# Kernel tuning notes

Hardware: AMD Instinct MI355X
Metric: run time of the kernel (lower is better)

## Reference

```python
import jax, jax.numpy as jnp
import numpy as np

B_SCALE = 1.3195079565048218
N_LEVELS = 16
BASE_RES = 16
MAX_PARAMS = 2 ** 19
N_POINTS = 1048576
PRIMES = (1, 2654435761, 805459861)  # uint32 hash primes (Instant-NGP)


def _level_meta():
    offsets, sizes, inds = [], [], []
    off = 0
    for i in range(N_LEVELS):
        res = int(np.ceil(BASE_RES * np.exp(i * np.log(B_SCALE)) - 1.0)) + 1
        p = res ** 3
        if p % 8 != 0:
            p = ((p + 7) // 8) * 8
        p = min(MAX_PARAMS, p)
        offsets.append(off)
        sizes.append(p)
        inds.append(res ** 3 <= p)  # dense (under_hash) vs hashed level
        off += p
    return offsets, sizes, inds, off


OFFSETS, SIZES, INDICATORS, TOTAL_PARAMS = _level_meta()
TOTAL_HASH_SIZE = TOTAL_PARAMS * 2  # == 11445040


def _encode_level(x01, table2, level):
    # x01: [N,3] in [0,1]; table2: [total_params, 2]
    scale = np.float32(BASE_RES * np.exp(level * np.log(B_SCALE)) - 1.0)
    resolution = np.uint32(np.ceil(scale) + 1)
    map_size = np.uint32(SIZES[level])
    pos = x01 * scale + 0.5
    grid_f = jnp.floor(pos)
    frac = pos - grid_f                           # [N,3] trilinear weights
    grid = grid_f.astype(jnp.uint32)              # [N,3]
    feat = jnp.zeros((x01.shape[0], 2), dtype=table2.dtype)
    primes = np.array(PRIMES, dtype=np.uint32)
    stride = np.array([1, int(resolution), int(resolution) * int(resolution)], dtype=np.uint32)
    for idx in range(8):  # 8 grid corners
        sel = np.array([(idx >> d) & 1 for d in range(3)], dtype=np.uint32)
        corner = grid + sel                       # [N,3] uint32
        w = jnp.prod(jnp.where(sel[None, :] == 1, frac, 1.0 - frac), axis=-1)  # [N]
        if INDICATORS[level]:
            c = corner * stride[None, :]
            h = c[:, 0] + c[:, 1] + c[:, 2]       # under_hash (dense indexing)
        else:
            c = corner * primes[None, :]          # uint32 wraparound multiply
            h = c[:, 0] ^ c[:, 1] ^ c[:, 2]       # fast_hash
        index = (h % map_size).astype(jnp.int32) + np.int32(OFFSETS[level])
        feat = feat + w[:, None] * table2[index]  # gather + trilinear blend
    return feat


def setup_inputs() -> dict:
    key = jax.random.key(0)
    k1, k2 = jax.random.split(key)
    positions = jax.random.uniform(k1, (N_POINTS, 3), dtype=jnp.float32, minval=-1.0, maxval=1.0)
    # random_initialize: (rand*2-1)*1e-4
    hash_table = jax.random.uniform(k2, (TOTAL_HASH_SIZE,), dtype=jnp.float32, minval=-1e-4, maxval=1e-4)
    return {"positions": positions, "hash_table": hash_table}


def reference(positions, hash_table):
    x01 = (positions + 1.0) * 0.5  # bound = 1
    table2 = hash_table.reshape(-1, 2)
    feats = [_encode_level(x01, table2, l) for l in range(N_LEVELS)]
    return jnp.concatenate(feats, axis=-1)  # [N, 32]
```

## Files before the change

kernel.cpp:

```cpp
#include <hip/hip_runtime.h>
#include <math.h>
#include <stdint.h>

#define NLV 16
#define NDENSE 6
#define NHASH 10
#define SORT_RES 32
#define NBINS (SORT_RES * SORT_RES * SORT_RES)

typedef float evf2 __attribute__((ext_vector_type(2)));
typedef unsigned int evu4 __attribute__((ext_vector_type(4)));

struct Params {
  float scale[NLV];
  uint32_t res[NLV];
  uint32_t msize[NLV];
  uint32_t offset[NLV];
};

struct ParamsD {
  float scale[NDENSE];
  uint32_t res[NDENSE];
  uint32_t msize[NDENSE];
  uint32_t offset[NDENSE];
};

__device__ __forceinline__ float ntload(const float* p) {
  return __builtin_nontemporal_load(p);
}

__device__ __forceinline__ uint32_t cell_key(float xr, float yr, float zr) {
  float x01 = (xr + 1.0f) * 0.5f;
  float y01 = (yr + 1.0f) * 0.5f;
  float z01 = (zr + 1.0f) * 0.5f;
  int cx = (int)(x01 * (float)SORT_RES);
  int cy = (int)(y01 * (float)SORT_RES);
  int cz = (int)(z01 * (float)SORT_RES);
  cx = cx < 0 ? 0 : (cx > SORT_RES-1 ? SORT_RES-1 : cx);
  cy = cy < 0 ? 0 : (cy > SORT_RES-1 ? SORT_RES-1 : cy);
  cz = cz < 0 ? 0 : (cz > SORT_RES-1 ? SORT_RES-1 : cz);
  return (uint32_t)(cx | (cy << 5) | (cz << 10));
}

__global__ __launch_bounds__(256) void zero_bins_kernel(uint32_t* bins) {
  int i = blockIdx.x * 256 + threadIdx.x;
  if (i < NBINS) bins[i] = 0u;
}

__global__ __launch_bounds__(256) void hist_kernel(
    const float* __restrict__ positions, uint32_t* __restrict__ bins, int n) {
  int t = blockIdx.x * 256 + threadIdx.x;
  int p0 = t * 4;
  if (p0 >= n) return;
  const float4 A = *reinterpret_cast<const float4*>(positions + 3*p0);
  const float4 B = *reinterpret_cast<const float4*>(positions + 3*p0 + 4);
  const float4 C = *reinterpret_cast<const float4*>(positions + 3*p0 + 8);
  atomicAdd(&bins[cell_key(A.x, A.y, A.z)], 1u);
  atomicAdd(&bins[cell_key(A.w, B.x, B.y)], 1u);
  atomicAdd(&bins[cell_key(B.z, B.w, C.x)], 1u);
  atomicAdd(&bins[cell_key(C.y, C.z, C.w)], 1u);
}

__global__ __launch_bounds__(1024) void scan_kernel(
    const uint32_t* __restrict__ bins, uint32_t* __restrict__ cursor) {
  __shared__ uint32_t lds[1024];
  int t = threadIdx.x;
  uint32_t local[32];
  uint32_t s = 0;
  #pragma unroll
  for (int j = 0; j < 32; ++j) { local[j] = bins[t*32 + j]; s += local[j]; }
  lds[t] = s;
  __syncthreads();
  for (int off = 1; off < 1024; off <<= 1) {
    uint32_t v = (t >= off) ? lds[t - off] : 0u;
    __syncthreads();
    lds[t] += v;
    __syncthreads();
  }
  uint32_t run = lds[t] - s;
  #pragma unroll
  for (int j = 0; j < 32; ++j) { cursor[t*32 + j] = run; run += local[j]; }
}

__global__ __launch_bounds__(256) void scatter_kernel(
    const float* __restrict__ positions, uint32_t* __restrict__ cursor,
    evu4* __restrict__ spi, int n) {
  int t = blockIdx.x * 256 + threadIdx.x;
  int p0 = t * 4;
  if (p0 >= n) return;
  const float4 A = *reinterpret_cast<const float4*>(positions + 3*p0);
  const float4 B = *reinterpret_cast<const float4*>(positions + 3*p0 + 4);
  const float4 C = *reinterpret_cast<const float4*>(positions + 3*p0 + 8);
  float xs[4] = {A.x, A.w, B.z, C.y};
  float ys[4] = {A.y, B.x, B.w, C.z};
  float zs[4] = {A.z, B.y, C.x, C.w};
  #pragma unroll
  for (int q = 0; q < 4; ++q) {
    uint32_t k = cell_key(xs[q], ys[q], zs[q]);
    uint32_t dst = atomicAdd(&cursor[k], 1u);
    evu4 v;
    v.x = __float_as_uint(xs[q]);
    v.y = __float_as_uint(ys[q]);
    v.z = __float_as_uint(zs[q]);
    v.w = (uint32_t)(p0 + q);
    spi[dst] = v;
  }
}

__global__ __launch_bounds__(256) void hash_level_kernel(
    const evu4* __restrict__ spi,
    const float* __restrict__ tbl,
    float2* __restrict__ tmp,
    float scale, uint32_t mask, int n)
{
  int t = blockIdx.x * 256 + threadIdx.x;
  int p0 = t * 2;
  if (p0 >= n) return;

  evu4 a = __builtin_nontemporal_load(spi + p0);
  evu4 b = (p0 + 1 < n) ? __builtin_nontemporal_load(spi + p0 + 1) : a;
  float xx[2] = {__uint_as_float(a.x), __uint_as_float(b.x)};
  float yy[2] = {__uint_as_float(a.y), __uint_as_float(b.y)};
  float zz[2] = {__uint_as_float(a.z), __uint_as_float(b.z)};

  float r0[2], r1[2];
  #pragma unroll
  for (int q = 0; q < 2; ++q) {
    float x = (xx[q] + 1.0f) * 0.5f;
    float y = (yy[q] + 1.0f) * 0.5f;
    float z = (zz[q] + 1.0f) * 0.5f;

    float px = x * scale + 0.5f;
    float py = y * scale + 0.5f;
    float pz = z * scale + 0.5f;
    float fx = floorf(px), fy = floorf(py), fz = floorf(pz);
    float tx = px - fx, ty = py - fy, tz = pz - fz;
    uint32_t gx = (uint32_t)fx, gy = (uint32_t)fy, gz = (uint32_t)fz;

    float wxa = 1.0f - tx, wxb = tx;
    float wy_[2] = {1.0f - ty, ty};
    float wz_[2] = {1.0f - tz, tz};

    float f0 = 0.0f, f1 = 0.0f;

    if ((gx & 1u) == 0u) {
      #pragma unroll
      for (int cyz = 0; cyz < 4; ++cyz) {
        uint32_t cy = gy + (cyz & 1u);
        uint32_t cz = gz + (cyz >> 1);
        uint32_t hy = (cy * 2654435761u) ^ (cz * 805459861u);
        uint32_t ha = (gx ^ hy) & mask;
        float wyz = wy_[cyz & 1u] * wz_[cyz >> 1];
        float wa = wxa * wyz, wb = wxb * wyz;
        const float4 t4 = *reinterpret_cast<const float4*>(tbl + 2u * (ha & ~1u));
        float2 ta, tb;
        if (ha & 1u) { ta.x = t4.z; ta.y = t4.w; tb.x = t4.x; tb.y = t4.y; }
        else         { ta.x = t4.x; ta.y = t4.y; tb.x = t4.z; tb.y = t4.w; }
        f0 += wa * ta.x; f1 += wa * ta.y;
        f0 += wb * tb.x; f1 += wb * tb.y;
      }
    } else {
      #pragma unroll
      for (int cyz = 0; cyz < 4; ++cyz) {
        uint32_t cy = gy + (cyz & 1u);
        uint32_t cz = gz + (cyz >> 1);
        uint32_t hy = (cy * 2654435761u) ^ (cz * 805459861u);
        uint32_t ha = (gx ^ hy) & mask;
        uint32_t hb = ((gx + 1u) ^ hy) & mask;
        float wyz = wy_[cyz & 1u] * wz_[cyz >> 1];
        float wa = wxa * wyz, wb = wxb * wyz;
        const float2 ta = *reinterpret_cast<const float2*>(tbl + 2u * ha);
        const float2 tb = *reinterpret_cast<const float2*>(tbl + 2u * hb);
        f0 += wa * ta.x; f1 += wa * ta.y;
        f0 += wb * tb.x; f1 += wb * tb.y;
      }
    }
    r0[q] = f0; r1[q] = f1;
  }

  evf2 v0; v0.x = r0[0]; v0.y = r1[0];
  __builtin_nontemporal_store(v0, reinterpret_cast<evf2*>(tmp + p0));
  if (p0 + 1 < n) {
    evf2 v1; v1.x = r0[1]; v1.y = r1[1];
    __builtin_nontemporal_store(v1, reinterpret_cast<evf2*>(tmp + p0 + 1));
  }
}

__global__ __launch_bounds__(256) void dense_pack2_kernel(
    const evu4* __restrict__ spi,
    const float* __restrict__ table,
    const float2* __restrict__ tmp,
    float* __restrict__ out,
    ParamsD prm, int n)
{
  __shared__ float lds[256 * 33];
  __shared__ uint32_t lds_oi[256];
  int t = threadIdx.x;
  int base = blockIdx.x * 256;
  int p = base + t;

  if (p < n) {
    evu4 a = __builtin_nontemporal_load(spi + p);
    float x = (__uint_as_float(a.x) + 1.0f) * 0.5f;
    float y = (__uint_as_float(a.y) + 1.0f) * 0.5f;
    float z = (__uint_as_float(a.z) + 1.0f) * 0.5f;
    lds_oi[t] = a.w;

    #pragma unroll
    for (int l = 0; l < NDENSE; ++l) {
      const float s = prm.scale[l];
      const uint32_t res = prm.res[l];
      const uint32_t ms = prm.msize[l];
      const float* __restrict__ tbl = table + 2u * prm.offset[l];
      const uint32_t res2 = res * res;

      float px = x * s + 0.5f;
      float py = y * s + 0.5f;
      float pz = z * s + 0.5f;
      float fx = floorf(px), fy = floorf(py), fz = floorf(pz);
      float tx = px - fx, ty = py - fy, tz = pz - fz;
      uint32_t gx = (uint32_t)fx, gy = (uint32_t)fy, gz = (uint32_t)fz;

      float wxa = 1.0f - tx, wxb = tx;
      float wy_[2] = {1.0f - ty, ty};
      float wz_[2] = {1.0f - tz, tz};

      float f0 = 0.0f, f1 = 0.0f;
      #pragma unroll
      for (int cyz = 0; cyz < 4; ++cyz) {
        uint32_t cy = gy + (cyz & 1u);
        uint32_t cz = gz + ((cyz >> 1) & 1u);
        uint32_t h = gx + cy * res + cz * res2;
        if (h >= ms) h -= ms;
        float wyz = wy_[cyz & 1u] * wz_[(cyz >> 1) & 1u];
        float2 ta, tb;
        if (h + 1u < ms) {
          const float4 t4 = *reinterpret_cast<const float4*>(tbl + 2u * h);
          ta.x = t4.x; ta.y = t4.y; tb.x = t4.z; tb.y = t4.w;
        } else {
          ta = *reinterpret_cast<const float2*>(tbl + 2u * h);
          tb = *reinterpret_cast<const float2*>(tbl);
        }
        float wa = wxa * wyz, wb = wxb * wyz;
        f0 += wa * ta.x; f1 += wa * ta.y;
        f0 += wb * tb.x; f1 += wb * tb.y;
      }
      lds[t*33 + 2*l]     = f0;
      lds[t*33 + 2*l + 1] = f1;
    }

    #pragma unroll
    for (int j = 0; j < NHASH; ++j) {
      evf2 v = __builtin_nontemporal_load(
          reinterpret_cast<const evf2*>(tmp + (size_t)j * n + p));
      lds[t*33 + 12 + 2*j]     = v.x;
      lds[t*33 + 12 + 2*j + 1] = v.y;
    }
  }
  __syncthreads();

  if (base + 256 <= n) {
    int qr = t >> 3, r = t & 7;
    #pragma unroll
    for (int k = 0; k < 8; ++k) {
      int q = k * 32 + qr;
      uint32_t oi = lds_oi[q];
      float4 v = make_float4(lds[q*33 + r*4], lds[q*33 + r*4 + 1],
                             lds[q*33 + r*4 + 2], lds[q*33 + r*4 + 3]);
      reinterpret_cast<float4*>(out + (size_t)oi * 32u)[r] = v;
    }
  } else if (p < n) {
    uint32_t oi = lds_oi[t];
    float4* o = reinterpret_cast<float4*>(out + (size_t)oi * 32u);
    #pragma unroll
    for (int k = 0; k < 8; ++k)
      o[k] = make_float4(lds[t*33 + 4*k], lds[t*33 + 4*k + 1],
                         lds[t*33 + 4*k + 2], lds[t*33 + 4*k + 3]);
  }
}

__global__ __launch_bounds__(256) void hash_level_unsorted_kernel(
    const float* __restrict__ positions,
    const float* __restrict__ tbl,
    float2* __restrict__ tmp,
    float scale, uint32_t mask, int n)
{
  int t = blockIdx.x * 256 + threadIdx.x;
  int p0 = t * 2;
  if (p0 >= n) return;

  float xx[2], yy[2], zz[2];
  {
    evf2 a = __builtin_nontemporal_load(reinterpret_cast<const evf2*>(positions + 3*p0));
    evf2 b = __builtin_nontemporal_load(reinterpret_cast<const evf2*>(positions + 3*p0 + 2));
    evf2 c = __builtin_nontemporal_load(reinterpret_cast<const evf2*>(positions + 3*p0 + 4));
    xx[0] = a.x; yy[0] = a.y; zz[0] = b.x;
    xx[1] = b.y; yy[1] = c.x; zz[1] = c.y;
  }

  float r0[2], r1[2];
  #pragma unroll
  for (int q = 0; q < 2; ++q) {
    float x = (xx[q] + 1.0f) * 0.5f;
    float y = (yy[q] + 1.0f) * 0.5f;
    float z = (zz[q] + 1.0f) * 0.5f;
    float px = x * scale + 0.5f;
    float py = y * scale + 0.5f;
    float pz = z * scale + 0.5f;
    float fx = floorf(px), fy = floorf(py), fz = floorf(pz);
    float tx = px - fx, ty = py - fy, tz = pz - fz;
    uint32_t gx = (uint32_t)fx, gy = (uint32_t)fy, gz = (uint32_t)fz;
    float wxa = 1.0f - tx, wxb = tx;
    float wy_[2] = {1.0f - ty, ty};
    float wz_[2] = {1.0f - tz, tz};
    float f0 = 0.0f, f1 = 0.0f;
    #pragma unroll
    for (int cyz = 0; cyz < 4; ++cyz) {
      uint32_t cy = gy + (cyz & 1u);
      uint32_t cz = gz + (cyz >> 1);
      uint32_t hy = (cy * 2654435761u) ^ (cz * 805459861u);
      uint32_t ha = (gx ^ hy) & mask;
      uint32_t hb = ((gx + 1u) ^ hy) & mask;
      float wyz = wy_[cyz & 1u] * wz_[cyz >> 1];
      float wa = wxa * wyz, wb = wxb * wyz;
      const float2 ta = *reinterpret_cast<const float2*>(tbl + 2u * ha);
      const float2 tb = *reinterpret_cast<const float2*>(tbl + 2u * hb);
      f0 += wa * ta.x; f1 += wa * ta.y;
      f0 += wb * tb.x; f1 += wb * tb.y;
    }
    r0[q] = f0; r1[q] = f1;
  }
  evf2 v0; v0.x = r0[0]; v0.y = r1[0];
  __builtin_nontemporal_store(v0, reinterpret_cast<evf2*>(tmp + p0));
  if (p0 + 1 < n) {
    evf2 v1; v1.x = r0[1]; v1.y = r1[1];
    __builtin_nontemporal_store(v1, reinterpret_cast<evf2*>(tmp + p0 + 1));
  }
}

__global__ __launch_bounds__(256) void dense_unsorted_kernel(
    const float* __restrict__ positions,
    const float* __restrict__ table,
    float2* __restrict__ tmp,
    ParamsD prm, int n)
{
  int p = blockIdx.x * 256 + threadIdx.x;
  if (p >= n) return;

  float x = (ntload(positions + 3*p+0) + 1.0f) * 0.5f;
  float y = (ntload(positions + 3*p+1) + 1.0f) * 0.5f;
  float z = (ntload(positions + 3*p+2) + 1.0f) * 0.5f;

  #pragma unroll
  for (int l = 0; l < NDENSE; ++l) {
    const float s = prm.scale[l];
    const uint32_t res = prm.res[l];
    const uint32_t ms = prm.msize[l];
    const float* __restrict__ tbl = table + 2u * prm.offset[l];
    const uint32_t res2 = res * res;
    float px = x * s + 0.5f;
    float py = y * s + 0.5f;
    float pz = z * s + 0.5f;
    float fx = floorf(px), fy = floorf(py), fz = floorf(pz);
    float tx = px - fx, ty = py - fy, tz = pz - fz;
    uint32_t gx = (uint32_t)fx, gy = (uint32_t)fy, gz = (uint32_t)fz;
    float wxa = 1.0f - tx, wxb = tx;
    float wy_[2] = {1.0f - ty, ty};
    float wz_[2] = {1.0f - tz, tz};
    float f0 = 0.0f, f1 = 0.0f;
    #pragma unroll
    for (int cyz = 0; cyz < 4; ++cyz) {
      uint32_t cy = gy + (cyz & 1u);
      uint32_t cz = gz + ((cyz >> 1) & 1u);
      uint32_t h = gx + cy * res + cz * res2;
      if (h >= ms) h -= ms;
      float wyz = wy_[cyz & 1u] * wz_[(cyz >> 1) & 1u];
      float2 ta, tb;
      if (h + 1u < ms) {
        const float4 t4 = *reinterpret_cast<const float4*>(tbl + 2u * h);
        ta.x = t4.x; ta.y = t4.y; tb.x = t4.z; tb.y = t4.w;
      } else {
        ta = *reinterpret_cast<const float2*>(tbl + 2u * h);
        tb = *reinterpret_cast<const float2*>(tbl);
      }
      float wa = wxa * wyz, wb = wxb * wyz;
      f0 += wa * ta.x; f1 += wa * ta.y;
      f0 += wb * tb.x; f1 += wb * tb.y;
    }
    evf2 v; v.x = f0; v.y = f1;
    __builtin_nontemporal_store(v,
        reinterpret_cast<evf2*>(tmp + (size_t)(NHASH + l) * n + p));
  }
}

__global__ __launch_bounds__(256) void stream_pack_kernel(
    const float2* __restrict__ tmp, float* __restrict__ out, int n)
{
  int p = blockIdx.x * 256 + threadIdx.x;
  if (p >= n) return;
  evf2 dv[NDENSE];
  #pragma unroll
  for (int j = 0; j < NDENSE; ++j)
    dv[j] = __builtin_nontemporal_load(
        reinterpret_cast<const evf2*>(tmp + (size_t)(NHASH + j) * n + p));
  evf2 hv[NHASH];
  #pragma unroll
  for (int j = 0; j < NHASH; ++j)
    hv[j] = __builtin_nontemporal_load(
        reinterpret_cast<const evf2*>(tmp + (size_t)j * n + p));
  float4* o = reinterpret_cast<float4*>(out + (size_t)p * 32u);
  #pragma unroll
  for (int j = 0; j < 3; ++j)
    o[j] = make_float4(dv[2*j].x, dv[2*j].y, dv[2*j+1].x, dv[2*j+1].y);
  #pragma unroll
  for (int j = 0; j < 5; ++j)
    o[3 + j] = make_float4(hv[2*j].x, hv[2*j].y, hv[2*j+1].x, hv[2*j+1].y);
}

__global__ __launch_bounds__(256) void hash_enc_kernel(
    const float* __restrict__ positions,
    const float* __restrict__ table,
    float* __restrict__ out,
    Params prm, int n)
{
  int p = blockIdx.x * 256 + threadIdx.x;
  if (p >= n) return;

  float x = (positions[3*p+0] + 1.0f) * 0.5f;
  float y = (positions[3*p+1] + 1.0f) * 0.5f;
  float z = (positions[3*p+2] + 1.0f) * 0.5f;

  float acc[32];

  #pragma unroll
  for (int l = 0; l < NLV; ++l) {
    const float s = prm.scale[l];
    const uint32_t res = prm.res[l];
    const uint32_t ms = prm.msize[l];
    const uint32_t off = prm.offset[l];
    float px = x * s + 0.5f;
    float py = y * s + 0.5f;
    float pz = z * s + 0.5f;
    float fx = floorf(px), fy = floorf(py), fz = floorf(pz);
    float tx = px - fx, ty = py - fy, tz = pz - fz;
    uint32_t gx = (uint32_t)fx, gy = (uint32_t)fy, gz = (uint32_t)fz;
    float wx[2] = {1.0f - tx, tx};
    float wy[2] = {1.0f - ty, ty};
    float wz[2] = {1.0f - tz, tz};
    float f0 = 0.0f, f1 = 0.0f;
    #pragma unroll
    for (int c = 0; c < 8; ++c) {
      uint32_t cx = gx + (c & 1u);
      uint32_t cy = gy + ((c >> 1) & 1u);
      uint32_t cz = gz + ((c >> 2) & 1u);
      uint32_t h;
      if (l < NDENSE) {
        h = cx + cy * res + cz * res * res;
        if (h >= ms) h -= ms;
      } else {
        h = cx ^ (cy * 2654435761u) ^ (cz * 805459861u);
        h &= (ms - 1u);
      }
      float w = (wx[c & 1u] * wy[(c >> 1) & 1u]) * wz[(c >> 2) & 1u];
      const float2 t = *reinterpret_cast<const float2*>(table + 2u * (h + off));
      f0 += w * t.x;
      f1 += w * t.y;
    }
    acc[2*l]   = f0;
    acc[2*l+1] = f1;
  }

  float4* o = reinterpret_cast<float4*>(out + (size_t)p * 32u);
  #pragma unroll
  for (int k = 0; k < 8; ++k)
    o[k] = make_float4(acc[4*k+0], acc[4*k+1], acc[4*k+2], acc[4*k+3]);
}

extern "C" void kernel_launch(void* const* d_in, const int* in_sizes, int n_in,
                              void* d_out, int out_size, void* d_ws, size_t ws_size,
                              hipStream_t stream) {
  const float* positions = (const float*)d_in[0];
  const float* table     = (const float*)d_in[1];
  float* out             = (float*)d_out;
  int n = in_sizes[0] / 3;

  Params prm;
  const double lnb = log(1.3195079565048218);
  uint32_t off = 0;
  for (int l = 0; l < NLV; ++l) {
    double sd = 16.0 * exp((double)l * lnb) - 1.0;
    uint32_t res_meta = (uint32_t)ceil(sd) + 1u;
    uint64_t p3 = (uint64_t)res_meta * res_meta * res_meta;
    uint64_t ps = (p3 % 8ull) ? ((p3 + 7ull) / 8ull) * 8ull : p3;
    if (ps > (1ull << 19)) ps = 1ull << 19;
    float sf = (float)sd;
    uint32_t res_enc = (uint32_t)(ceilf(sf) + 1.0f);
    prm.scale[l]  = sf;
    prm.res[l]    = res_enc;
    prm.msize[l]  = (uint32_t)ps;
    prm.offset[l] = off;
    off += (uint32_t)ps;
  }
  ParamsD pd;
  for (int l = 0; l < NDENSE; ++l) {
    pd.scale[l] = prm.scale[l]; pd.res[l] = prm.res[l];
    pd.msize[l] = prm.msize[l]; pd.offset[l] = prm.offset[l];
  }

  dim3 block(256);
  dim3 gfull((n + 255) / 256);
  dim3 ghash((n/2 + 255) / 256);
  dim3 gquad((n/4 + 255) / 256);

  size_t tmp_b  = (size_t)NHASH * n * sizeof(float2);
  size_t sp_off = tmp_b;
  size_t bn_off = sp_off + (size_t)n * sizeof(evu4);
  size_t cu_off = bn_off + (size_t)NBINS * sizeof(uint32_t);
  size_t total  = cu_off + (size_t)NBINS * sizeof(uint32_t);
  size_t ws16   = (size_t)NLV * n * sizeof(float2);

  char* wsb = (char*)d_ws;

  if (ws_size >= total && (n % 4) == 0) {
    float2*   tmp    = (float2*)wsb;
    evu4*     spi    = (evu4*)(wsb + sp_off);
    uint32_t* bins   = (uint32_t*)(wsb + bn_off);
    uint32_t* cursor = (uint32_t*)(wsb + cu_off);

    hipLaunchKernelGGL(zero_bins_kernel, dim3((NBINS + 255) / 256), block, 0, stream, bins);
    hipLaunchKernelGGL(hist_kernel, gquad, block, 0, stream, positions, bins, n);
    hipLaunchKernelGGL(scan_kernel, dim3(1), dim3(1024), 0, stream, bins, cursor);
    hipLaunchKernelGGL(scatter_kernel, gquad, block, 0, stream,
                       positions, cursor, spi, n);

    for (int l = NDENSE; l < NLV; ++l) {
      hipLaunchKernelGGL(hash_level_kernel, ghash, block, 0, stream,
                         spi, table + 2u * prm.offset[l],
                         tmp + (size_t)(l - NDENSE) * n,
                         prm.scale[l], prm.msize[l] - 1u, n);
    }
    hipLaunchKernelGGL(dense_pack2_kernel, gfull, block, 0, stream,
                       spi, table, tmp, out, pd, n);
  } else if (ws_size >= ws16 && (n % 2) == 0) {
    float2* tmp = (float2*)d_ws;
    for (int l = NDENSE; l < NLV; ++l) {
      hipLaunchKernelGGL(hash_level_unsorted_kernel, ghash, block, 0, stream,
                         positions, table + 2u * prm.offset[l],
                         tmp + (size_t)(l - NDENSE) * n,
                         prm.scale[l], prm.msize[l] - 1u, n);
    }
    hipLaunchKernelGGL(dense_unsorted_kernel, gfull, block, 0, stream,
                       positions, table, tmp, pd, n);
    hipLaunchKernelGGL(stream_pack_kernel, gfull, block, 0, stream,
                       tmp, out, n);
  } else {
    hipLaunchKernelGGL(hash_enc_kernel, gfull, block, 0, stream,
                       positions, table, out, prm, n);
  }
}
```

Measured before the change: 436.2 us.

## Store hashed-level features in fp16, scatter indices only, shrink pack blocks

Intermediate per-level hash features are now stored as half-precision pairs instead of float2, halving the temporary write/read traffic between the hash-level kernels and the pack kernel. The scatter kernel writes only a 4-byte index per point, and a new materialize kernel gathers the sorted positions into the 16-byte records. The pack kernel block size drops to 128 threads to cut LDS use per block and raise occupancy. The fp16 rounding of features (values around 1e-4, some in the subnormal range) costs precision and may exceed tolerance, and the extra materialize pass adds a gather over the positions.

```diff
diff --git a/kernel.cpp b/kernel.cpp
--- a/kernel.cpp
+++ b/kernel.cpp
@@ -10,6 +10,7 @@
 
 typedef float evf2 __attribute__((ext_vector_type(2)));
 typedef unsigned int evu4 __attribute__((ext_vector_type(4)));
+typedef _Float16 evh2 __attribute__((ext_vector_type(2)));
 
 struct Params {
   float scale[NLV];
@@ -84,7 +85,7 @@
 
 __global__ __launch_bounds__(256) void scatter_kernel(
     const float* __restrict__ positions, uint32_t* __restrict__ cursor,
-    evu4* __restrict__ spi, int n) {
+    uint32_t* __restrict__ sidx, int n) {
   int t = blockIdx.x * 256 + threadIdx.x;
   int p0 = t * 4;
   if (p0 >= n) return;
@@ -98,19 +99,28 @@
   for (int q = 0; q < 4; ++q) {
     uint32_t k = cell_key(xs[q], ys[q], zs[q]);
     uint32_t dst = atomicAdd(&cursor[k], 1u);
-    evu4 v;
-    v.x = __float_as_uint(xs[q]);
-    v.y = __float_as_uint(ys[q]);
-    v.z = __float_as_uint(zs[q]);
-    v.w = (uint32_t)(p0 + q);
-    spi[dst] = v;
-  }
+    sidx[dst] = (uint32_t)(p0 + q);
+  }
+}
+
+__global__ __launch_bounds__(256) void materialize_kernel(
+    const float* __restrict__ positions, const uint32_t* __restrict__ sidx,
+    evu4* __restrict__ spi, int n) {
+  int p = blockIdx.x * 256 + threadIdx.x;
+  if (p >= n) return;
+  uint32_t si = sidx[p];
+  evu4 v;
+  v.x = __float_as_uint(positions[3*si]);
+  v.y = __float_as_uint(positions[3*si + 1]);
+  v.z = __float_as_uint(positions[3*si + 2]);
+  v.w = si;
+  spi[p] = v;
 }
 
 __global__ __launch_bounds__(256) void hash_level_kernel(
     const evu4* __restrict__ spi,
     const float* __restrict__ tbl,
-    float2* __restrict__ tmp,
+    evh2* __restrict__ tmpH,
     float scale, uint32_t mask, int n)
 {
   int t = blockIdx.x * 256 + threadIdx.x;
@@ -178,25 +188,26 @@
     r0[q] = f0; r1[q] = f1;
   }
 
-  evf2 v0; v0.x = r0[0]; v0.y = r1[0];
-  __builtin_nontemporal_store(v0, reinterpret_cast<evf2*>(tmp + p0));
+  evh2 v0; v0.x = (_Float16)r0[0]; v0.y = (_Float16)r1[0];
+  __builtin_nontemporal_store(v0, tmpH + p0);
   if (p0 + 1 < n) {
-    evf2 v1; v1.x = r0[1]; v1.y = r1[1];
-    __builtin_nontemporal_store(v1, reinterpret_cast<evf2*>(tmp + p0 + 1));
-  }
-}
-
-__global__ __launch_bounds__(256) void dense_pack2_kernel(
+    evh2 v1; v1.x = (_Float16)r0[1]; v1.y = (_Float16)r1[1];
+    __builtin_nontemporal_store(v1, tmpH + p0 + 1);
+  }
+}
+
+#define PBS 128
+__global__ __launch_bounds__(PBS) void dense_pack2_kernel(
     const evu4* __restrict__ spi,
     const float* __restrict__ table,
-    const float2* __restrict__ tmp,
+    const evh2* __restrict__ tmpH,
     float* __restrict__ out,
     ParamsD prm, int n)
 {
-  __shared__ float lds[256 * 33];
-  __shared__ uint32_t lds_oi[256];
+  __shared__ float lds[PBS * 33];
+  __shared__ uint32_t lds_oi[PBS];
   int t = threadIdx.x;
-  int base = blockIdx.x * 256;
+  int base = blockIdx.x * PBS;
   int p = base + t;
 
   if (p < n) {
@@ -251,19 +262,18 @@
 
     #pragma unroll
     for (int j = 0; j < NHASH; ++j) {
-      evf2 v = __builtin_nontemporal_load(
-          reinterpret_cast<const evf2*>(tmp + (size_t)j * n + p));
-      lds[t*33 + 12 + 2*j]     = v.x;
-      lds[t*33 + 12 + 2*j + 1] = v.y;
+      evh2 v = __builtin_nontemporal_load(tmpH + (size_t)j * n + p);
+      lds[t*33 + 12 + 2*j]     = (float)v.x;
+      lds[t*33 + 12 + 2*j + 1] = (float)v.y;
     }
   }
   __syncthreads();
 
-  if (base + 256 <= n) {
+  if (base + PBS <= n) {
     int qr = t >> 3, r = t & 7;
     #pragma unroll
     for (int k = 0; k < 8; ++k) {
-      int q = k * 32 + qr;
+      int q = k * (PBS/8) + qr;
       uint32_t oi = lds_oi[q];
       float4 v = make_float4(lds[q*33 + r*4], lds[q*33 + r*4 + 1],
                              lds[q*33 + r*4 + 2], lds[q*33 + r*4 + 3]);
@@ -511,10 +521,12 @@
   dim3 gfull((n + 255) / 256);
   dim3 ghash((n/2 + 255) / 256);
   dim3 gquad((n/4 + 255) / 256);
-
-  size_t tmp_b  = (size_t)NHASH * n * sizeof(float2);
+  dim3 gpack((n + PBS - 1) / PBS);
+
+  size_t tmp_b  = (size_t)NHASH * n * sizeof(evh2);
   size_t sp_off = tmp_b;
-  size_t bn_off = sp_off + (size_t)n * sizeof(evu4);
+  size_t si_off = sp_off + (size_t)n * sizeof(evu4);
+  size_t bn_off = si_off + (size_t)n * sizeof(uint32_t);
   size_t cu_off = bn_off + (size_t)NBINS * sizeof(uint32_t);
   size_t total  = cu_off + (size_t)NBINS * sizeof(uint32_t);
   size_t ws16   = (size_t)NLV * n * sizeof(float2);
@@ -522,8 +534,9 @@
   char* wsb = (char*)d_ws;
 
   if (ws_size >= total && (n % 4) == 0) {
-    float2*   tmp    = (float2*)wsb;
+    evh2*     tmpH   = (evh2*)wsb;
     evu4*     spi    = (evu4*)(wsb + sp_off);
+    uint32_t* sidx   = (uint32_t*)(wsb + si_off);
     uint32_t* bins   = (uint32_t*)(wsb + bn_off);
     uint32_t* cursor = (uint32_t*)(wsb + cu_off);
 
@@ -531,16 +544,18 @@
     hipLaunchKernelGGL(hist_kernel, gquad, block, 0, stream, positions, bins, n);
     hipLaunchKernelGGL(scan_kernel, dim3(1), dim3(1024), 0, stream, bins, cursor);
     hipLaunchKernelGGL(scatter_kernel, gquad, block, 0, stream,
-                       positions, cursor, spi, n);
+                       positions, cursor, sidx, n);
+    hipLaunchKernelGGL(materialize_kernel, gfull, block, 0, stream,
+                       positions, sidx, spi, n);
 
     for (int l = NDENSE; l < NLV; ++l) {
       hipLaunchKernelGGL(hash_level_kernel, ghash, block, 0, stream,
                          spi, table + 2u * prm.offset[l],
-                         tmp + (size_t)(l - NDENSE) * n,
+                         tmpH + (size_t)(l - NDENSE) * n,
                          prm.scale[l], prm.msize[l] - 1u, n);
     }
-    hipLaunchKernelGGL(dense_pack2_kernel, gfull, block, 0, stream,
-                       spi, table, tmp, out, pd, n);
+    hipLaunchKernelGGL(dense_pack2_kernel, gpack, dim3(PBS), 0, stream,
+                       spi, table, tmpH, out, pd, n);
   } else if (ws_size >= ws16 && (n % 2) == 0) {
     float2* tmp = (float2*)d_ws;
     for (int l = NDENSE; l < NLV; ++l) {
```

Measured after the change: 444.9 us. 1.02x slower.
